# Performance work log

Hardware: AMD Instinct MI355X
Metric: run time of the kernel (lower is better)

Reference implementation:

```python
import jax, jax.numpy as jnp
import numpy as np

IN_F = 4096
OUT_F = 11008
GROUPSIZE = 128
N_GROUPS = IN_F // GROUPSIZE  # 32


def setup_inputs() -> dict:
    key = jax.random.key(0)
    k1, k2, k3, k4 = jax.random.split(key, 4)
    x = jax.random.normal(k1, (4, 2048, IN_F), dtype=jnp.float32)
    # packed 4-bit weights: 8 nibbles per int32 along the input dim
    qweight = jax.random.randint(k2, (IN_F // 8, OUT_F), 0, 2**31 - 1, dtype=jnp.int32)
    # packed 4-bit zero points: 8 nibbles per int32 along the output dim
    qzeros = jax.random.randint(k3, (N_GROUPS, OUT_F // 8), 0, 2**31 - 1, dtype=jnp.int32)
    scales = jax.random.uniform(k4, (N_GROUPS, OUT_F), dtype=jnp.float32,
                                minval=0.001, maxval=0.01)
    g_idx = (jnp.arange(IN_F, dtype=jnp.int32) // GROUPSIZE).astype(jnp.int32)
    return {"x": x, "qweight": qweight, "scales": scales,
            "qzeros": qzeros, "g_idx": g_idx}


def _dequantize(qweight, scales, qzeros, g_idx):
    """GPTQ v2 dequant: W[i, j] = scales[g_idx[i], j] * (q[i, j] - (z[g_idx[i], j] + 1))."""
    shifts = jnp.arange(8, dtype=jnp.int32) * 4  # nibble shift amounts
    # unpack weights along input dim: [in/8, 8, out] -> [in, out]
    q = (qweight[:, None, :] >> shifts[None, :, None]) & 0xF
    q = q.reshape(-1, qweight.shape[1]).astype(scales.dtype)
    # unpack zeros along output dim: [g, out/8, 8] -> [g, out]; +1 per GPTQ v2
    z = ((qzeros[:, :, None] >> shifts[None, None, :]) & 0xF) + 1
    z = z.reshape(qzeros.shape[0], -1).astype(scales.dtype)
    return scales[g_idx] * (q - z[g_idx])  # [in, out]


def reference(x, qweight, scales, qzeros, g_idx):
    W = _dequantize(qweight, scales, qzeros, g_idx)  # [IN_F, OUT_F]
    return jnp.einsum('bsi,io->bso', x, W)
```

## Files before the change

### kernel.cpp

```cpp
#include <hip/hip_runtime.h>
#include <hip/hip_bf16.h>

#define IN_F 4096
#define OUT_F 11008

typedef __bf16 bf16_t;
typedef _Float16 f16_t;
typedef f16_t f16x8 __attribute__((ext_vector_type(8)));
typedef f16_t f16x2 __attribute__((ext_vector_type(2)));
typedef u_int32_t u32;
typedef u32 u32x4 __attribute__((ext_vector_type(4)));
typedef bf16_t bf16x8 __attribute__((ext_vector_type(8)));
typedef float f32x4 __attribute__((ext_vector_type(4)));

__global__ __launch_bounds__(256) void cvt_x_kernel(const float* __restrict__ x,
                                                    f16_t* __restrict__ xb) {
    size_t i = ((size_t)blockIdx.x * 256 + threadIdx.x) * 8;
    f32x4 v0 = __builtin_nontemporal_load((const f32x4*)(x + i));
    f32x4 v1 = __builtin_nontemporal_load((const f32x4*)(x + i + 4));
    f16x8 h;
    h[0]=(f16_t)v0[0]; h[1]=(f16_t)v0[1]; h[2]=(f16_t)v0[2]; h[3]=(f16_t)v0[3];
    h[4]=(f16_t)v1[0]; h[5]=(f16_t)v1[1]; h[6]=(f16_t)v1[2]; h[7]=(f16_t)v1[3];
    *(f16x8*)(xb + i) = h;
}


#define NI (IN_F / 128)

__global__ __launch_bounds__(512, 2) void gemm_q4(const f16_t* __restrict__ A,
                                                  const int* __restrict__ qweight,
                                                  const float* __restrict__ scales,
                                                  const int* __restrict__ qzeros,
                                                  float* __restrict__ C) {
    __shared__ __align__(16) f16_t smemA[2 * 2 * 128 * 64];
    __shared__ __align__(16) u32   smemB[2 * 2048];

    const int tid  = threadIdx.x;
    const int lane = tid & 63;
    const int wid  = tid >> 6;
    const int wr   = wid >> 2;
    const int wc   = wid & 3;

    const int bid = blockIdx.x;
    const int swz = (bid & 7) * 172 + (bid >> 3);
    const int bx = swz % 43;
    const int by = swz / 43;
    const int m0 = by * 256;
    const int n0 = bx * 256;

    int lr0, kb0, lr1, kb1;
    {
        int L0 = tid * 16;
        int p0 = L0 ^ (((L0 >> 7) & 7) << 4);
        lr0 = p0 >> 7; kb0 = (p0 & 127) >> 1;
        int L1 = (512 + tid) * 16;
        int p1 = L1 ^ (((L1 >> 7) & 7) << 4);
        lr1 = p1 >> 7; kb1 = (p1 & 127) >> 1;
    }

    const int xm = (lane & 7) << 4;
    const int arow = lane & 15;
    int colk[2];
    #pragma unroll
    for (int ks = 0; ks < 2; ++ks)
        colk[ks] = ((ks * 64) + ((lane >> 4) * 16)) ^ xm;

    const int ncol = n0 + wc * 64 + (lane & 15);
    const u32* bw = smemB + (wc * 512 + (lane >> 4) * 16 + (lane & 15));
    const int kwS  = (tid >> 2) & 7;
    const int colS = (tid >> 5) * 16 + (tid & 3) * 4;
    const u32* qB = (const u32*)qweight + (size_t)kwS * OUT_F + n0 + colS;
    const int zsh = (lane & 7) * 4;

#define STAGE_A(buf, half, koff)                                                           \
    do {                                                                                   \
        const f16_t* g0_ = A + (size_t)(m0 + (half) * 128 + lr0) * IN_F + (koff) + kb0;    \
        __builtin_amdgcn_global_load_lds(                                                  \
            (const __attribute__((address_space(1))) u32*)g0_,                             \
            (__attribute__((address_space(3))) u32*)((char*)smemA + (buf) * 32768 +        \
                                                     (half) * 16384 + wid * 1024),         \
            16, 0, 0);                                                                     \
        const f16_t* g1_ = A + (size_t)(m0 + (half) * 128 + lr1) * IN_F + (koff) + kb1;    \
        __builtin_amdgcn_global_load_lds(                                                  \
            (const __attribute__((address_space(1))) u32*)g1_,                             \
            (__attribute__((address_space(3))) u32*)((char*)smemA + (buf) * 32768 +        \
                                                     (half) * 16384 + 8192 + wid * 1024),  \
            16, 0, 0);                                                                     \
    } while (0)

#define STAGE_B(buf, ktrow)                                                                \
    __builtin_amdgcn_global_load_lds(                                                      \
        (const __attribute__((address_space(1))) u32*)(qB + (size_t)(ktrow) * OUT_F),      \
        (__attribute__((address_space(3))) u32*)((char*)smemB + (buf) * 8192 + tid * 16),  \
        16, 0, 0)

#define RD_A(dst, buf, mbase)                                                              \
    _Pragma("unroll") for (int mm = 0; mm < 4; ++mm)                                       \
    _Pragma("unroll") for (int ks = 0; ks < 2; ++ks)                                       \
        dst[mm * 2 + ks] = *(const f16x8*)((const char*)smemA + (buf) * 32768 +            \
            wr * 16384 + (((mbase) + mm) * 16 + arow) * 128 + colk[ks]);

#define RD_W(buf)                                                                          \
    _Pragma("unroll") for (int nt = 0; nt < 4; ++nt)                                       \
    _Pragma("unroll") for (int ks = 0; ks < 2; ++ks)                                       \
        w[nt * 2 + ks] = bw[(buf) * 2048 + nt * 128 + ks * 64];

#define DEQ(dst, nt0)                                                                      \
    _Pragma("unroll") for (int nn = 0; nn < 2; ++nn)                                       \
    _Pragma("unroll") for (int ks = 0; ks < 2; ++ks) {                                     \
        const u32 wv_ = w[((nt0) + nn) * 2 + ks];                                          \
        const u32 od_ = wv_ >> 4;                                                          \
        const f16x2 zp_ = zh[(nt0) + nn];                                                  \
        const f16x2 sp_ = sh[(nt0) + nn];                                                  \
        u32x4 hw_;                                                                         \
        _Pragma("unroll") for (int p = 0; p < 4; ++p) {                                    \
            u32 t_ = __builtin_amdgcn_perm(od_, wv_,                                       \
                         0x0C000C00u | (u32)p | ((u32)(4 + p) << 16));                     \
            u32 u_ = (t_ & 0x000F000Fu) | 0x64006400u;                                     \
            f16x2 b_ = (__builtin_bit_cast(f16x2, u_) - zp_) * sp_;                        \
            hw_[p] = __builtin_bit_cast(u32, b_);                                          \
        }                                                                                  \
        dst[nn * 2 + ks] = __builtin_bit_cast(f16x8, hw_);                                 \
    }

#define MFMA_Q(aArr, bArr, mbase, nbase)                                                   \
    __builtin_amdgcn_s_setprio(1);                                                         \
    _Pragma("unroll") for (int mm = 0; mm < 4; ++mm)                                       \
    _Pragma("unroll") for (int nn = 0; nn < 2; ++nn)                                       \
    _Pragma("unroll") for (int ks = 0; ks < 2; ++ks)                                       \
        acc[(mbase) + mm][(nbase) + nn] = __builtin_amdgcn_mfma_f32_16x16x32_f16(          \
            aArr[mm * 2 + ks], bArr[nn * 2 + ks], acc[(mbase) + mm][(nbase) + nn],         \
            0, 0, 0);                                                                      \
    __builtin_amdgcn_s_setprio(0);

#define CVT_SCALES()                                                                       \
    _Pragma("unroll") for (int nt = 0; nt < 4; ++nt) {                                     \
        u32 zb_ = 0x6401u + ((zraw[nt] >> zsh) & 0xFu);                                    \
        zb_ |= zb_ << 16;                                                                  \
        zh[nt] = __builtin_bit_cast(f16x2, zb_);                                           \
        u32 sb_ = (u32)__builtin_bit_cast(unsigned short, (f16_t)sraw[nt]);                \
        sb_ |= sb_ << 16;                                                                  \
        sh[nt] = __builtin_bit_cast(f16x2, sb_);                                           \
    }

#define SCHED0() __builtin_amdgcn_sched_barrier(0)
#define BAR() do { SCHED0(); __builtin_amdgcn_s_barrier(); } while (0)
#define VMCNT10() asm volatile("s_waitcnt vmcnt(10)" ::: "memory")
#define VMCNT2()  asm volatile("s_waitcnt vmcnt(2)"  ::: "memory")
#define VMCNT0()  asm volatile("s_waitcnt vmcnt(0)"  ::: "memory")

    f32x4 acc[8][4];
    #pragma unroll
    for (int m = 0; m < 8; ++m)
        #pragma unroll
        for (int n = 0; n < 4; ++n)
            acc[m][n] = (f32x4)0.0f;

    f16x8 aR[8], b01[4], b23[4];
    u32   w[8];
    f16x2 zh[4], sh[4];
    float sraw[4]; u32 zraw[4];

    STAGE_A(0, 0, 0); STAGE_A(0, 1, 0);
    STAGE_B(0, 0);
    STAGE_B(1, 8);
    STAGE_A(1, 0, 64);
    VMCNT0();
    BAR();
    #pragma unroll
    for (int nt = 0; nt < 4; ++nt) {
        sraw[nt] = scales[ncol + nt * 16];
        zraw[nt] = ((const u32*)qzeros)[(ncol >> 3) + nt * 2];
    }
    CVT_SCALES();
    RD_W(0);
    DEQ(b01, 0);
    DEQ(b23, 2);
    BAR();

    for (int i = 0; i < NI; ++i) {
        const int  kc = i * 128;
        const int  kn = kc + 128;
        const bool nl = (i + 1 < NI);

        RD_A(aR, 0, 0);
        STAGE_A(1, 1, kc + 64);
        if (nl) STAGE_B(0, (kn) >> 3);
        MFMA_Q(aR, b01, 0, 0);
        BAR();
        if (nl) {
            #pragma unroll
            for (int nt = 0; nt < 4; ++nt) {
                sraw[nt] = scales[ncol + (i + 1) * OUT_F + nt * 16];
                zraw[nt] = ((const u32*)qzeros)[(ncol >> 3) + (i + 1) * (OUT_F / 8) + nt * 2];
            }
        }
        MFMA_Q(aR, b23, 0, 2);
        BAR();
        RD_A(aR, 0, 4);
        MFMA_Q(aR, b01, 4, 0);
        BAR();
        if (nl) STAGE_A(0, 0, kn);
        MFMA_Q(aR, b23, 4, 2);
        if (nl) VMCNT10(); else VMCNT0();
        RD_W(1);
        DEQ(b01, 0);
        DEQ(b23, 2);
        BAR();
        RD_A(aR, 1, 0);
        if (nl) { STAGE_A(0, 1, kn); STAGE_B(1, (kn + 64) >> 3); }
        MFMA_Q(aR, b01, 0, 0);
        BAR();
        MFMA_Q(aR, b23, 0, 2);
        BAR();
        RD_A(aR, 1, 4);
        if (nl) CVT_SCALES();
        MFMA_Q(aR, b01, 4, 0);
        BAR();
        if (nl) STAGE_A(1, 0, kn + 64);
        MFMA_Q(aR, b23, 4, 2);
        if (nl) VMCNT2(); else VMCNT0();
        if (nl) {
            RD_W(0);
            DEQ(b01, 0);
            DEQ(b23, 2);
        }
        BAR();
    }

    const int cn  = lane & 15;
    const int cr4 = (lane >> 4) * 4;
    #pragma unroll
    for (int m = 0; m < 8; ++m) {
        #pragma unroll
        for (int r = 0; r < 4; ++r) {
            const int grow = m0 + wr * 128 + m * 16 + cr4 + r;
            float* orow = C + (size_t)grow * OUT_F + n0 + wc * 64 + cn;
            #pragma unroll
            for (int n = 0; n < 4; ++n)
                orow[n * 16] = acc[m][n][r];
        }
    }
}

#define BMf 128
#define BNf 128
#define BKf 32
#define LDPF 40

__global__ __launch_bounds__(256, 2) void gptq_gemm_fused(
    const float* __restrict__ x, const int* __restrict__ qweight,
    const float* __restrict__ scales, const int* __restrict__ qzeros,
    float* __restrict__ out)
{
    __shared__ bf16_t As[BMf * LDPF];
    __shared__ bf16_t Bs[BNf * LDPF];
    const int tid = threadIdx.x, lane = tid & 63, wid = tid >> 6;
    const int wr = wid >> 1, wc = wid & 1;
    const int m0 = blockIdx.y * BMf, n0 = blockIdx.x * BNf;
    const int a_row = tid >> 2, a_slot = tid & 3;
    const int b_k8l = tid >> 7, b_n = tid & 127;

    f32x4 acc[4][4];
    #pragma unroll
    for (int i = 0; i < 4; ++i)
        #pragma unroll
        for (int j = 0; j < 4; ++j) acc[i][j] = (f32x4)0.0f;

    for (int kt = 0; kt < IN_F / BKf; ++kt) {
        const int k0 = kt * BKf;
        const int g  = k0 >> 7;
        __syncthreads();
        #pragma unroll
        for (int p = 0; p < 2; ++p) {
            const int row = a_row + p * 64;
            const float* src = x + (size_t)(m0 + row) * IN_F + k0 + a_slot * 8;
            f32x4 v0 = *(const f32x4*)src;
            f32x4 v1 = *(const f32x4*)(src + 4);
            bf16x8 h;
            h[0]=(bf16_t)v0[0]; h[1]=(bf16_t)v0[1]; h[2]=(bf16_t)v0[2]; h[3]=(bf16_t)v0[3];
            h[4]=(bf16_t)v1[0]; h[5]=(bf16_t)v1[1]; h[6]=(bf16_t)v1[2]; h[7]=(bf16_t)v1[3];
            *(bf16x8*)(&As[row * LDPF + a_slot * 8]) = h;
        }
        {
            const int gn = n0 + b_n;
            const float s  = scales[(size_t)g * OUT_F + gn];
            const int   zw = qzeros[(size_t)g * (OUT_F / 8) + (gn >> 3)];
            const float sz = s * (float)(((zw >> ((gn & 7) * 4)) & 0xF) + 1);
            #pragma unroll
            for (int p = 0; p < 2; ++p) {
                const int k8l = b_k8l + p * 2;
                const int w = qweight[(size_t)(k0 / 8 + k8l) * OUT_F + gn];
                bf16x8 h;
                #pragma unroll
                for (int j = 0; j < 8; ++j)
                    h[j] = (bf16_t)fmaf((float)((w >> (4 * j)) & 0xF), s, -sz);
                *(bf16x8*)(&Bs[b_n * LDPF + k8l * 8]) = h;
            }
        }
        __syncthreads();
        bf16x8 af[4], bfr[4];
        #pragma unroll
        for (int m = 0; m < 4; ++m)
            af[m] = *(const bf16x8*)(&As[(wr * 64 + m * 16 + (lane & 15)) * LDPF + (lane >> 4) * 8]);
        #pragma unroll
        for (int n = 0; n < 4; ++n)
            bfr[n] = *(const bf16x8*)(&Bs[(wc * 64 + n * 16 + (lane & 15)) * LDPF + (lane >> 4) * 8]);
        #pragma unroll
        for (int m = 0; m < 4; ++m)
            #pragma unroll
            for (int n = 0; n < 4; ++n)
                acc[m][n] = __builtin_amdgcn_mfma_f32_16x16x32_bf16(af[m], bfr[n], acc[m][n], 0, 0, 0);
    }
    const int cn = lane & 15, cr4 = (lane >> 4) * 4;
    #pragma unroll
    for (int m = 0; m < 4; ++m)
        #pragma unroll
        for (int r = 0; r < 4; ++r) {
            const int grow = m0 + wr * 64 + m * 16 + cr4 + r;
            float* orow = out + (size_t)grow * OUT_F + n0 + wc * 64 + cn;
            #pragma unroll
            for (int n = 0; n < 4; ++n) orow[n * 16] = acc[m][n][r];
        }
}

extern "C" void kernel_launch(void* const* d_in, const int* in_sizes, int n_in,
                              void* d_out, int out_size, void* d_ws, size_t ws_size,
                              hipStream_t stream) {
    const float* x       = (const float*)d_in[0];
    const int*   qweight = (const int*)d_in[1];
    const float* scales  = (const float*)d_in[2];
    const int*   qzeros  = (const int*)d_in[3];
    float* out = (float*)d_out;

    const int M = in_sizes[0] / IN_F;
    const size_t xb_bytes = (size_t)M * IN_F * 2;

    if (ws_size >= xb_bytes && (M % 256) == 0) {
        f16_t* xb = (f16_t*)d_ws;
        cvt_x_kernel<<<dim3((M * IN_F) / (256 * 8)), dim3(256), 0, stream>>>(x, xb);
        const int nwg = (OUT_F / 256) * (M / 256);
        gemm_q4<<<dim3(nwg), dim3(512), 0, stream>>>(xb, qweight, scales, qzeros, out);
    } else {
        gptq_gemm_fused<<<dim3(OUT_F / BNf, M / BMf), dim3(256), 0, stream>>>(
            x, qweight, scales, qzeros, out);
    }
}
```

Before: 812.2 us.

## Double-buffer A fragments and single-buffer dequantized B to interleave dequant with MFMA

Switches the register allocation from one A fragment set plus two dequantized B sets to two A fragment sets (top and bottom M halves) plus one B set. Each half of the dequantized weights is now produced just before it is consumed, and those dequant steps are interleaved between MFMA groups. The goal is to hide dequant ALU work behind matrix ops and to spread LDS reads across the loop. The tradeoff is a reordered MFMA sequence that sits inside tight barrier and vmcnt dependencies, and the liveness of the staged buffers has to stay correct after the reordering.

Result: slower. 975.2 us (+20.1%).

```diff
diff --git a/kernel.cpp b/kernel.cpp
--- a/kernel.cpp
+++ b/kernel.cpp
@@ -105,7 +105,7 @@
     _Pragma("unroll") for (int ks = 0; ks < 2; ++ks)                                       \
         w[nt * 2 + ks] = bw[(buf) * 2048 + nt * 128 + ks * 64];
 
-#define DEQ(dst, nt0)                                                                      \
+#define DEQ(nt0)                                                                           \
     _Pragma("unroll") for (int nn = 0; nn < 2; ++nn)                                       \
     _Pragma("unroll") for (int ks = 0; ks < 2; ++ks) {                                     \
         const u32 wv_ = w[((nt0) + nn) * 2 + ks];                                          \
@@ -120,16 +120,16 @@
             f16x2 b_ = (__builtin_bit_cast(f16x2, u_) - zp_) * sp_;                        \
             hw_[p] = __builtin_bit_cast(u32, b_);                                          \
         }                                                                                  \
-        dst[nn * 2 + ks] = __builtin_bit_cast(f16x8, hw_);                                 \
-    }
-
-#define MFMA_Q(aArr, bArr, mbase, nbase)                                                   \
+        bP[nn * 2 + ks] = __builtin_bit_cast(f16x8, hw_);                                  \
+    }
+
+#define MFMA_Q(aArr, mbase, nbase)                                                         \
     __builtin_amdgcn_s_setprio(1);                                                         \
     _Pragma("unroll") for (int mm = 0; mm < 4; ++mm)                                       \
     _Pragma("unroll") for (int nn = 0; nn < 2; ++nn)                                       \
     _Pragma("unroll") for (int ks = 0; ks < 2; ++ks)                                       \
         acc[(mbase) + mm][(nbase) + nn] = __builtin_amdgcn_mfma_f32_16x16x32_f16(          \
-            aArr[mm * 2 + ks], bArr[nn * 2 + ks], acc[(mbase) + mm][(nbase) + nn],         \
+            aArr[mm * 2 + ks], bP[nn * 2 + ks], acc[(mbase) + mm][(nbase) + nn],           \
             0, 0, 0);                                                                      \
     __builtin_amdgcn_s_setprio(0);
 
@@ -156,7 +156,7 @@
         for (int n = 0; n < 4; ++n)
             acc[m][n] = (f32x4)0.0f;
 
-    f16x8 aR[8], b01[4], b23[4];
+    f16x8 aX[8], aY[8], bP[4];
     u32   w[8];
     f16x2 zh[4], sh[4];
     float sraw[4]; u32 zraw[4];
@@ -174,8 +174,8 @@
     }
     CVT_SCALES();
     RD_W(0);
-    DEQ(b01, 0);
-    DEQ(b23, 2);
+    DEQ(0);
+    RD_A(aX, 0, 0);
     BAR();
 
     for (int i = 0; i < NI; ++i) {
@@ -183,10 +183,10 @@
         const int  kn = kc + 128;
         const bool nl = (i + 1 < NI);
 
-        RD_A(aR, 0, 0);
+        RD_A(aY, 0, 4);
         STAGE_A(1, 1, kc + 64);
-        if (nl) STAGE_B(0, (kn) >> 3);
-        MFMA_Q(aR, b01, 0, 0);
+        if (nl) STAGE_B(0, kn >> 3);
+        MFMA_Q(aX, 0, 0);
         BAR();
         if (nl) {
             #pragma unroll
@@ -195,35 +195,35 @@
                 zraw[nt] = ((const u32*)qzeros)[(ncol >> 3) + (i + 1) * (OUT_F / 8) + nt * 2];
             }
         }
-        MFMA_Q(aR, b23, 0, 2);
-        BAR();
-        RD_A(aR, 0, 4);
-        MFMA_Q(aR, b01, 4, 0);
+        MFMA_Q(aY, 4, 0);
+        DEQ(2);
+        BAR();
+        RD_W(1);
+        MFMA_Q(aX, 0, 2);
         BAR();
         if (nl) STAGE_A(0, 0, kn);
-        MFMA_Q(aR, b23, 4, 2);
+        MFMA_Q(aY, 4, 2);
         if (nl) VMCNT10(); else VMCNT0();
-        RD_W(1);
-        DEQ(b01, 0);
-        DEQ(b23, 2);
-        BAR();
-        RD_A(aR, 1, 0);
+        RD_A(aX, 1, 0);
+        DEQ(0);
+        BAR();
+        RD_A(aY, 1, 4);
         if (nl) { STAGE_A(0, 1, kn); STAGE_B(1, (kn + 64) >> 3); }
-        MFMA_Q(aR, b01, 0, 0);
-        BAR();
-        MFMA_Q(aR, b23, 0, 2);
-        BAR();
-        RD_A(aR, 1, 4);
+        MFMA_Q(aX, 0, 0);
+        BAR();
+        MFMA_Q(aY, 4, 0);
+        DEQ(2);
+        BAR();
         if (nl) CVT_SCALES();
-        MFMA_Q(aR, b01, 4, 0);
+        MFMA_Q(aX, 0, 2);
         BAR();
         if (nl) STAGE_A(1, 0, kn + 64);
-        MFMA_Q(aR, b23, 4, 2);
+        MFMA_Q(aY, 4, 2);
         if (nl) VMCNT2(); else VMCNT0();
         if (nl) {
+            RD_A(aX, 0, 0);
             RD_W(0);
-            DEQ(b01, 0);
-            DEQ(b23, 2);
+            DEQ(0);
         }
         BAR();
     }
```
